# Performance work log

Hardware: AMD Instinct MI355X
Metric: run time of the kernel (lower is better)

Reference implementation:

```python
import jax, jax.numpy as jnp
import numpy as np

B, T, IN_DIM, H_DIM = 64, 512, 512, 1024


def setup_inputs() -> dict:
    key = jax.random.key(0)
    ks = jax.random.split(key, 10)
    s_in = 1.0 / np.sqrt(IN_DIM)
    s_h = 1.0 / np.sqrt(H_DIM)
    return {
        "inputs": jax.random.normal(ks[0], (B, T, IN_DIM), jnp.float32),
        "Wxr": jax.random.normal(ks[1], (H_DIM, IN_DIM), jnp.float32) * s_in,
        "bxr": jax.random.normal(ks[2], (H_DIM,), jnp.float32) * s_in,
        "Whr": jax.random.normal(ks[3], (H_DIM, H_DIM), jnp.float32) * s_h,
        "Wxz": jax.random.normal(ks[4], (H_DIM, IN_DIM), jnp.float32) * s_in,
        "bxz": jax.random.normal(ks[5], (H_DIM,), jnp.float32) * s_in,
        "Whz": jax.random.normal(ks[6], (H_DIM, H_DIM), jnp.float32) * s_h,
        "Wxn": jax.random.normal(ks[7], (H_DIM, IN_DIM), jnp.float32) * s_in,
        "bxn": jax.random.normal(ks[8], (H_DIM,), jnp.float32) * s_in,
        "Whn": jax.random.normal(ks[9], (H_DIM, H_DIM), jnp.float32) * s_h,
    }


def reference(inputs, Wxr, bxr, Whr, Wxz, bxz, Whz, Wxn, bxn, Whn):
    # Precompute all input projections in batched GEMMs: [B,T,H]
    xr = jnp.einsum("bti,hi->bth", inputs, Wxr) + bxr
    xz = jnp.einsum("bti,hi->bth", inputs, Wxz) + bxz
    xn = jnp.einsum("bti,hi->bth", inputs, Wxn) + bxn
    # time-major for scan: [T,B,H]
    xs = (xr.transpose(1, 0, 2), xz.transpose(1, 0, 2), xn.transpose(1, 0, 2))

    def step(h, x):
        xr_t, xz_t, xn_t = x
        r = jax.nn.sigmoid(xr_t + h @ Whr.T)
        z = jax.nn.sigmoid(xz_t + h @ Whz.T)
        n = jnp.tanh(xn_t + r * (h @ Whn.T))
        h_new = (1.0 - z) * n + z * h
        return h_new, h_new

    h0 = jnp.zeros((inputs.shape[0], Wxr.shape[0]), inputs.dtype)
    h_last, hs = jax.lax.scan(step, h0, xs)
    hidden_states = hs.transpose(1, 0, 2)  # [B,T,H] (batch_first)
    # dropout p=0 -> identity
    return (h_last, hidden_states)
```

## Files before the change

kernel.cpp:

```cpp
#include <hip/hip_runtime.h>

typedef __attribute__((ext_vector_type(8))) short short8;
typedef __attribute__((ext_vector_type(4))) float f32x4;

#define TT 512
#define HD 1024
#define BD 64
#define NWG 256

union U16B { short8 s; unsigned long long u[2]; };

__device__ __forceinline__ unsigned short f2bf(float f) {
  unsigned u = __float_as_uint(f);
  u += 0x7fffu + ((u >> 16) & 1u);
  return (unsigned short)(u >> 16);
}

__global__ void prep_xt(const float* __restrict__ x, short8* __restrict__ XT) {
  const int bid = blockIdx.x;
  const int b = bid >> 9;
  const int t = bid & 511;
  const int tid = threadIdx.x;
  const float* src = x + ((size_t)(b * TT + t)) * 512 + tid * 8;
  const f32x4* s4 = (const f32x4*)src;
  f32x4 lo = s4[0], hi = s4[1];
  short8 o;
#pragma unroll
  for (int j = 0; j < 4; ++j) {
    o[j] = (short)f2bf(lo[j]);
    o[4 + j] = (short)f2bf(hi[j]);
  }
  const int bt = b >> 4, m = b & 15, ks = tid >> 2, q = tid & 3;
  XT[(((size_t)bt * TT + t) * 16 + ks) * 64 + q * 16 + m] = o;
}

__global__ __launch_bounds__(256, 1) void gru_main(
    const float* __restrict__ Wxr, const float* __restrict__ bxr,
    const float* __restrict__ Whr,
    const float* __restrict__ Wxz, const float* __restrict__ bxz,
    const float* __restrict__ Whz,
    const float* __restrict__ Wxn, const float* __restrict__ bxn,
    const float* __restrict__ Whn,
    const short8* __restrict__ XT, short* __restrict__ HF,
    unsigned* __restrict__ bar, float* __restrict__ out) {
  extern __shared__ char lds[];
  short8* wh = (short8*)lds;
  short8* wx = (short8*)(lds + 98304);
  float* red = (float*)(lds + 147456);

  const int wg = blockIdx.x;
  const int bt = wg & 3;
  const int ct = wg >> 2;
  const int c0 = ct << 4;
  const int tid = threadIdx.x;
  const int wv = tid >> 6;
  const int lane = tid & 63;

  for (int idx = tid; idx < 3 * 32 * 64; idx += 256) {
    const int g = idx >> 11, rem = idx & 2047, ks = rem >> 6, ln = rem & 63;
    const float* W = (g == 0) ? Whr : (g == 1) ? Whz : Whn;
    const float* src = W + (size_t)(c0 + (ln & 15)) * HD + ks * 32 + (ln >> 4) * 8;
    short8 v;
#pragma unroll
    for (int j = 0; j < 8; ++j) v[j] = (short)f2bf(src[j]);
    wh[idx] = v;
  }
  for (int idx = tid; idx < 3 * 16 * 64; idx += 256) {
    const int g = idx >> 10, rem = idx & 1023, ks = rem >> 6, ln = rem & 63;
    const float* W = (g == 0) ? Wxr : (g == 1) ? Wxz : Wxn;
    const float* src = W + (size_t)(c0 + (ln & 15)) * 512 + ks * 32 + (ln >> 4) * 8;
    short8 v;
#pragma unroll
    for (int j = 0; j < 8; ++j) v[j] = (short)f2bf(src[j]);
    wx[idx] = v;
  }
  __syncthreads();

  const int c_off = tid & 15, b_off = tid >> 4;
  const int c = c0 + c_off;
  const int b = (bt << 4) + b_off;
  const float br_ = bxr[c], bz_ = bxz[c], bn_ = bxn[c];
  float h_old = 0.f;

  const int hf_elem = (((bt * 32 + (c >> 5)) * 64) + ((c >> 3) & 3) * 16 + b_off) * 8 + (c & 7);
  const int rl = ((b_off >> 2) << 4) + c_off;
  const int rr = b_off & 3;

  unsigned* flags = bar + bt * 256;
  const unsigned long long* fl =
      (const unsigned long long*)(flags + lane * 4);

  float* out_hlast = out;
  float* out_hidden = out + BD * HD;

  for (int t = 0; t < TT; ++t) {
    const int p = t & 1;

    const short8* xrd = XT + (((size_t)bt * TT + t) * 16 + (wv << 2)) * 64 + lane;
    short8 xa[4];
#pragma unroll
    for (int kk = 0; kk < 4; ++kk) xa[kk] = xrd[kk * 64];

    f32x4 aR = {0.f, 0.f, 0.f, 0.f};
    f32x4 aZ = {0.f, 0.f, 0.f, 0.f};
    f32x4 aNh = {0.f, 0.f, 0.f, 0.f};
    f32x4 aNx = {0.f, 0.f, 0.f, 0.f};
#pragma unroll
    for (int kk = 0; kk < 4; ++kk) {
      const int ks = (wv << 2) + kk;
      aR = __builtin_amdgcn_mfma_f32_16x16x32_bf16(xa[kk], wx[(0 * 16 + ks) * 64 + lane], aR, 0, 0, 0);
      aZ = __builtin_amdgcn_mfma_f32_16x16x32_bf16(xa[kk], wx[(1 * 16 + ks) * 64 + lane], aZ, 0, 0, 0);
      aNx = __builtin_amdgcn_mfma_f32_16x16x32_bf16(xa[kk], wx[(2 * 16 + ks) * 64 + lane], aNx, 0, 0, 0);
    }

    if (t) {
      const unsigned tt = (unsigned)t;
      for (;;) {
        unsigned long long a0 = __hip_atomic_load(fl, __ATOMIC_RELAXED, __HIP_MEMORY_SCOPE_AGENT);
        unsigned long long a1 = __hip_atomic_load(fl + 1, __ATOMIC_RELAXED, __HIP_MEMORY_SCOPE_AGENT);
        const unsigned f0 = (unsigned)a0, f1 = (unsigned)(a0 >> 32);
        const unsigned f2 = (unsigned)a1, f3 = (unsigned)(a1 >> 32);
        const int ok = (f0 >= tt) & (f1 >= tt) & (f2 >= tt) & (f3 >= tt);
        if (__all(ok)) break;
      }
    }

    const unsigned long long* hfu = (const unsigned long long*)(HF + p * 65536);
    U16B ha[8];
#pragma unroll
    for (int kk = 0; kk < 8; ++kk) {
      const size_t u = (size_t)(bt * 32 + (wv << 3) + kk) * 64 + lane;
      ha[kk].u[0] = __hip_atomic_load(hfu + u * 2, __ATOMIC_RELAXED, __HIP_MEMORY_SCOPE_AGENT);
      ha[kk].u[1] = __hip_atomic_load(hfu + u * 2 + 1, __ATOMIC_RELAXED, __HIP_MEMORY_SCOPE_AGENT);
    }
#pragma unroll
    for (int kk = 0; kk < 8; ++kk) {
      const int ks = (wv << 3) + kk;
      aR = __builtin_amdgcn_mfma_f32_16x16x32_bf16(ha[kk].s, wh[(0 * 32 + ks) * 64 + lane], aR, 0, 0, 0);
      aZ = __builtin_amdgcn_mfma_f32_16x16x32_bf16(ha[kk].s, wh[(1 * 32 + ks) * 64 + lane], aZ, 0, 0, 0);
      aNh = __builtin_amdgcn_mfma_f32_16x16x32_bf16(ha[kk].s, wh[(2 * 32 + ks) * 64 + lane], aNh, 0, 0, 0);
    }

    {
      f32x4* r4 = (f32x4*)red;
      r4[(0 * 4 + wv) * 64 + lane] = aR;
      r4[(1 * 4 + wv) * 64 + lane] = aZ;
      r4[(2 * 4 + wv) * 64 + lane] = aNh;
      r4[(3 * 4 + wv) * 64 + lane] = aNx;
    }
    __syncthreads();
    float sR = 0.f, sZ = 0.f, sNh = 0.f, sNx = 0.f;
#pragma unroll
    for (int v = 0; v < 4; ++v) {
      sR += red[((0 * 4 + v) * 64 + rl) * 4 + rr];
      sZ += red[((1 * 4 + v) * 64 + rl) * 4 + rr];
      sNh += red[((2 * 4 + v) * 64 + rl) * 4 + rr];
      sNx += red[((3 * 4 + v) * 64 + rl) * 4 + rr];
    }

    const float r = 1.f / (1.f + __expf(-(sR + br_)));
    const float z = 1.f / (1.f + __expf(-(sZ + bz_)));
    float pre_n = sNx + bn_ + r * sNh;
    pre_n = fminf(fmaxf(pre_n, -30.f), 30.f);
    const float e2 = __expf(2.f * pre_n);
    const float n = (e2 - 1.f) / (e2 + 1.f);
    const float hn = (1.f - z) * n + z * h_old;
    h_old = hn;

    if (t < TT - 1) {
      __hip_atomic_store((unsigned short*)(HF + ((t + 1) & 1) * 65536 + hf_elem),
                         f2bf(hn), __ATOMIC_RELAXED, __HIP_MEMORY_SCOPE_AGENT);
      asm volatile("s_waitcnt vmcnt(0)" ::: "memory");
      if (lane == 0) {
        __hip_atomic_store(flags + ct * 4 + wv, (unsigned)(t + 1),
                           __ATOMIC_RELAXED, __HIP_MEMORY_SCOPE_AGENT);
      }
      out_hidden[((size_t)b * TT + t) * HD + c] = hn;
    } else {
      out_hidden[((size_t)b * TT + t) * HD + c] = hn;
      out_hlast[(size_t)b * HD + c] = hn;
    }
  }
}

extern "C" void kernel_launch(void* const* d_in, const int* in_sizes, int n_in,
                              void* d_out, int out_size, void* d_ws, size_t ws_size,
                              hipStream_t stream) {
  const float* inputs = (const float*)d_in[0];
  const float* Wxr = (const float*)d_in[1];
  const float* bxr = (const float*)d_in[2];
  const float* Whr = (const float*)d_in[3];
  const float* Wxz = (const float*)d_in[4];
  const float* bxz = (const float*)d_in[5];
  const float* Whz = (const float*)d_in[6];
  const float* Wxn = (const float*)d_in[7];
  const float* bxn = (const float*)d_in[8];
  const float* Whn = (const float*)d_in[9];
  float* out = (float*)d_out;

  char* ws = (char*)d_ws;
  short8* XT = (short8*)ws;
  short* HF = (short*)(ws + 33554432);
  unsigned* bar = (unsigned*)(ws + 33554432 + 262144);

  hipMemsetAsync(bar, 0, 4096, stream);
  hipMemsetAsync(HF, 0, 131072, stream);
  prep_xt<<<dim3(64 * 512), dim3(64), 0, stream>>>(inputs, XT);

  (void)hipFuncSetAttribute((const void*)gru_main,
                            hipFuncAttributeMaxDynamicSharedMemorySize, 163840);
  gru_main<<<dim3(NWG), dim3(256), 163840, stream>>>(
      Wxr, bxr, Whr, Wxz, bxz, Whz, Wxn, bxn, Whn, XT, HF, bar, out);
}
```

Baseline: 1.654 ms.

## Embed step tags in hidden-state words to replace separate flag barrier

Each 64-bit hidden-state slot now carries two bf16 values plus the timestep tag, so consumers poll the data itself instead of separate flag words. This removes the producer's vmcnt wait and the flag store, and it lets the h loads be issued before the input-projection MFMAs. The cost is four times more exchange memory, a shuffle to pack pairs, and an extra __syncthreads to protect the reduction buffer. If any tag mismatches, the whole fragment is reloaded, which can add polling traffic.

```diff
diff --git a/kernel.cpp b/kernel.cpp
--- a/kernel.cpp
+++ b/kernel.cpp
@@ -2,13 +2,14 @@
 
 typedef __attribute__((ext_vector_type(8))) short short8;
 typedef __attribute__((ext_vector_type(4))) float f32x4;
+typedef __attribute__((ext_vector_type(4))) unsigned int u32x4;
 
 #define TT 512
 #define HD 1024
 #define BD 64
 #define NWG 256
 
-union U16B { short8 s; unsigned long long u[2]; };
+union FRAG { u32x4 d; short8 s; };
 
 __device__ __forceinline__ unsigned short f2bf(float f) {
   unsigned u = __float_as_uint(f);
@@ -34,6 +35,8 @@
   XT[(((size_t)bt * TT + t) * 16 + ks) * 64 + q * 16 + m] = o;
 }
 
+#define PARQ ((size_t)(4 * 32 * 64 * 4))
+
 __global__ __launch_bounds__(256, 1) void gru_main(
     const float* __restrict__ Wxr, const float* __restrict__ bxr,
     const float* __restrict__ Whr,
@@ -41,8 +44,8 @@
     const float* __restrict__ Whz,
     const float* __restrict__ Wxn, const float* __restrict__ bxn,
     const float* __restrict__ Whn,
-    const short8* __restrict__ XT, short* __restrict__ HF,
-    unsigned* __restrict__ bar, float* __restrict__ out) {
+    const short8* __restrict__ XT, unsigned long long* __restrict__ HF,
+    float* __restrict__ out) {
   extern __shared__ char lds[];
   short8* wh = (short8*)lds;
   short8* wx = (short8*)(lds + 98304);
@@ -82,19 +85,29 @@
   const float br_ = bxr[c], bz_ = bxz[c], bn_ = bxn[c];
   float h_old = 0.f;
 
-  const int hf_elem = (((bt * 32 + (c >> 5)) * 64) + ((c >> 3) & 3) * 16 + b_off) * 8 + (c & 7);
   const int rl = ((b_off >> 2) << 4) + c_off;
   const int rr = b_off & 3;
 
-  unsigned* flags = bar + bt * 256;
-  const unsigned long long* fl =
-      (const unsigned long long*)(flags + lane * 4);
+  const size_t prod_li =
+      ((size_t)(bt * 32 + (c >> 5)) * 64 + ((c >> 3) & 3) * 16 + b_off) * 4 +
+      ((c & 7) >> 1);
+  const unsigned long long* cons_b =
+      HF + ((size_t)(bt * 32 + (wv << 3)) * 64 + lane) * 4;
 
   float* out_hlast = out;
   float* out_hidden = out + BD * HD;
 
   for (int t = 0; t < TT; ++t) {
     const int p = t & 1;
+    const unsigned long long* cb = cons_b + (size_t)p * PARQ;
+
+    unsigned long long L[8][4];
+#pragma unroll
+    for (int kk = 0; kk < 8; ++kk)
+#pragma unroll
+      for (int j = 0; j < 4; ++j)
+        L[kk][j] = __hip_atomic_load(cb + kk * 256 + j, __ATOMIC_RELAXED,
+                                     __HIP_MEMORY_SCOPE_AGENT);
 
     const short8* xrd = XT + (((size_t)bt * TT + t) * 16 + (wv << 2)) * 64 + lane;
     short8 xa[4];
@@ -113,32 +126,34 @@
       aNx = __builtin_amdgcn_mfma_f32_16x16x32_bf16(xa[kk], wx[(2 * 16 + ks) * 64 + lane], aNx, 0, 0, 0);
     }
 
-    if (t) {
-      const unsigned tt = (unsigned)t;
+    {
+      const unsigned tt_ = (unsigned)t;
       for (;;) {
-        unsigned long long a0 = __hip_atomic_load(fl, __ATOMIC_RELAXED, __HIP_MEMORY_SCOPE_AGENT);
-        unsigned long long a1 = __hip_atomic_load(fl + 1, __ATOMIC_RELAXED, __HIP_MEMORY_SCOPE_AGENT);
-        const unsigned f0 = (unsigned)a0, f1 = (unsigned)(a0 >> 32);
-        const unsigned f2 = (unsigned)a1, f3 = (unsigned)(a1 >> 32);
-        const int ok = (f0 >= tt) & (f1 >= tt) & (f2 >= tt) & (f3 >= tt);
-        if (__all(ok)) break;
+        unsigned bad = 0;
+#pragma unroll
+        for (int kk = 0; kk < 8; ++kk)
+#pragma unroll
+          for (int j = 0; j < 4; ++j)
+            bad |= ((unsigned)(L[kk][j] >> 32)) ^ tt_;
+        if (__all(bad == 0)) break;
+#pragma unroll
+        for (int kk = 0; kk < 8; ++kk)
+#pragma unroll
+          for (int j = 0; j < 4; ++j)
+            L[kk][j] = __hip_atomic_load(cb + kk * 256 + j, __ATOMIC_RELAXED,
+                                         __HIP_MEMORY_SCOPE_AGENT);
       }
     }
 
-    const unsigned long long* hfu = (const unsigned long long*)(HF + p * 65536);
-    U16B ha[8];
 #pragma unroll
     for (int kk = 0; kk < 8; ++kk) {
-      const size_t u = (size_t)(bt * 32 + (wv << 3) + kk) * 64 + lane;
-      ha[kk].u[0] = __hip_atomic_load(hfu + u * 2, __ATOMIC_RELAXED, __HIP_MEMORY_SCOPE_AGENT);
-      ha[kk].u[1] = __hip_atomic_load(hfu + u * 2 + 1, __ATOMIC_RELAXED, __HIP_MEMORY_SCOPE_AGENT);
-    }
-#pragma unroll
-    for (int kk = 0; kk < 8; ++kk) {
+      FRAG f;
+      f.d = (u32x4){(unsigned)L[kk][0], (unsigned)L[kk][1],
+                    (unsigned)L[kk][2], (unsigned)L[kk][3]};
       const int ks = (wv << 3) + kk;
-      aR = __builtin_amdgcn_mfma_f32_16x16x32_bf16(ha[kk].s, wh[(0 * 32 + ks) * 64 + lane], aR, 0, 0, 0);
-      aZ = __builtin_amdgcn_mfma_f32_16x16x32_bf16(ha[kk].s, wh[(1 * 32 + ks) * 64 + lane], aZ, 0, 0, 0);
-      aNh = __builtin_amdgcn_mfma_f32_16x16x32_bf16(ha[kk].s, wh[(2 * 32 + ks) * 64 + lane], aNh, 0, 0, 0);
+      aR = __builtin_amdgcn_mfma_f32_16x16x32_bf16(f.s, wh[(0 * 32 + ks) * 64 + lane], aR, 0, 0, 0);
+      aZ = __builtin_amdgcn_mfma_f32_16x16x32_bf16(f.s, wh[(1 * 32 + ks) * 64 + lane], aZ, 0, 0, 0);
+      aNh = __builtin_amdgcn_mfma_f32_16x16x32_bf16(f.s, wh[(2 * 32 + ks) * 64 + lane], aNh, 0, 0, 0);
     }
 
     {
@@ -157,6 +172,7 @@
       sNh += red[((2 * 4 + v) * 64 + rl) * 4 + rr];
       sNx += red[((3 * 4 + v) * 64 + rl) * 4 + rr];
     }
+    __syncthreads();
 
     const float r = 1.f / (1.f + __expf(-(sR + br_)));
     const float z = 1.f / (1.f + __expf(-(sZ + bz_)));
@@ -167,12 +183,15 @@
     const float hn = (1.f - z) * n + z * h_old;
     h_old = hn;
 
+    const unsigned hb = f2bf(hn);
+    const unsigned hb_hi = (unsigned)__shfl_down((int)hb, 1);
+
     if (t < TT - 1) {
-      __hip_atomic_store((unsigned short*)(HF + ((t + 1) & 1) * 65536 + hf_elem),
-                         f2bf(hn), __ATOMIC_RELAXED, __HIP_MEMORY_SCOPE_AGENT);
-      asm volatile("s_waitcnt vmcnt(0)" ::: "memory");
-      if (lane == 0) {
-        __hip_atomic_store(flags + ct * 4 + wv, (unsigned)(t + 1),
+      if (!(c_off & 1)) {
+        const unsigned long long val =
+            (unsigned long long)(hb | (hb_hi << 16)) |
+            ((unsigned long long)(unsigned)(t + 1) << 32);
+        __hip_atomic_store(HF + (size_t)((t + 1) & 1) * PARQ + prod_li, val,
                            __ATOMIC_RELAXED, __HIP_MEMORY_SCOPE_AGENT);
       }
       out_hidden[((size_t)b * TT + t) * HD + c] = hn;
@@ -200,15 +219,13 @@
 
   char* ws = (char*)d_ws;
   short8* XT = (short8*)ws;
-  short* HF = (short*)(ws + 33554432);
-  unsigned* bar = (unsigned*)(ws + 33554432 + 262144);
-
-  hipMemsetAsync(bar, 0, 4096, stream);
-  hipMemsetAsync(HF, 0, 131072, stream);
+  unsigned long long* HF = (unsigned long long*)(ws + 33554432);
+
+  hipMemsetAsync(HF, 0, 524288, stream);
   prep_xt<<<dim3(64 * 512), dim3(64), 0, stream>>>(inputs, XT);
 
   (void)hipFuncSetAttribute((const void*)gru_main,
                             hipFuncAttributeMaxDynamicSharedMemorySize, 163840);
   gru_main<<<dim3(NWG), dim3(256), 163840, stream>>>(
-      Wxr, bxr, Whr, Wxz, bxz, Whz, Wxn, bxn, Whn, XT, HF, bar, out);
-}
+      Wxr, bxr, Whr, Wxz, bxz, Whz, Wxn, bxn, Whn, XT, HF, out);
+}
```

Result: slower. 3.142 ms (+90.0%).

## Rewrite cross-workgroup wait as inline-asm poll-then-load with packed h stores

Applied to the files above, without the earlier changes.

Replaces the C++ flag-polling loop with an inline-assembly loop. Each lane polls one flag with two staggered in-flight loads, then issues the hidden-state dwordx4 loads right after the wait in the same asm block. Hidden-state writes are packed into 32-bit stores via a lane shuffle, halving the number of stores. Wh fragments are preloaded from LDS into registers before the wait, and a second __syncthreads is added to protect the reduction buffer. The goal is lower per-step barrier latency on the serial recurrence, at the cost of more register pressure and fragile hand-written asm.

```diff
diff --git a/kernel.cpp b/kernel.cpp
--- a/kernel.cpp
+++ b/kernel.cpp
@@ -2,13 +2,14 @@
 
 typedef __attribute__((ext_vector_type(8))) short short8;
 typedef __attribute__((ext_vector_type(4))) float f32x4;
+typedef __attribute__((ext_vector_type(4))) unsigned int u32x4;
 
 #define TT 512
 #define HD 1024
 #define BD 64
 #define NWG 256
 
-union U16B { short8 s; unsigned long long u[2]; };
+union FRAG { u32x4 d; short8 s; };
 
 __device__ __forceinline__ unsigned short f2bf(float f) {
   unsigned u = __float_as_uint(f);
@@ -34,6 +35,39 @@
   XT[(((size_t)bt * TT + t) * 16 + ks) * 64 + q * 16 + m] = o;
 }
 
+#define PARB ((size_t)131072)
+
+#define WAIT_AND_LOAD()                                                   \
+  asm volatile(                                                           \
+      "global_load_dword %8, %10, off sc0 sc1\n\t"                        \
+      "s_sleep 4\n\t"                                                     \
+      "global_load_dword %9, %10, off sc0 sc1\n\t"                        \
+      "1:\n\t"                                                            \
+      "s_waitcnt vmcnt(1)\n\t"                                            \
+      "v_cmp_gt_u32 vcc, %11, %8\n\t"                                     \
+      "s_cbranch_vccz 2f\n\t"                                             \
+      "global_load_dword %8, %10, off sc0 sc1\n\t"                        \
+      "s_waitcnt vmcnt(1)\n\t"                                            \
+      "v_cmp_gt_u32 vcc, %11, %9\n\t"                                     \
+      "s_cbranch_vccz 2f\n\t"                                             \
+      "global_load_dword %9, %10, off sc0 sc1\n\t"                        \
+      "s_branch 1b\n\t"                                                   \
+      "2:\n\t"                                                            \
+      "global_load_dwordx4 %0, %12, off sc0 sc1\n\t"                      \
+      "global_load_dwordx4 %1, %12, off offset:1024 sc0 sc1\n\t"          \
+      "global_load_dwordx4 %2, %12, off offset:2048 sc0 sc1\n\t"          \
+      "global_load_dwordx4 %3, %12, off offset:3072 sc0 sc1\n\t"          \
+      "global_load_dwordx4 %4, %13, off sc0 sc1\n\t"                      \
+      "global_load_dwordx4 %5, %13, off offset:1024 sc0 sc1\n\t"          \
+      "global_load_dwordx4 %6, %13, off offset:2048 sc0 sc1\n\t"          \
+      "global_load_dwordx4 %7, %13, off offset:3072 sc0 sc1\n\t"          \
+      "s_waitcnt vmcnt(0)"                                                \
+      : "=&v"(H[0]), "=&v"(H[1]), "=&v"(H[2]), "=&v"(H[3]),               \
+        "=&v"(H[4]), "=&v"(H[5]), "=&v"(H[6]), "=&v"(H[7]),               \
+        "=&v"(f0s), "=&v"(f1s)                                            \
+      : "v"(hint_p), "v"(tt_), "v"(p0), "v"(p1)                           \
+      : "vcc", "memory")
+
 __global__ __launch_bounds__(256, 1) void gru_main(
     const float* __restrict__ Wxr, const float* __restrict__ bxr,
     const float* __restrict__ Whr,
@@ -41,8 +75,8 @@
     const float* __restrict__ Whz,
     const float* __restrict__ Wxn, const float* __restrict__ bxn,
     const float* __restrict__ Whn,
-    const short8* __restrict__ XT, short* __restrict__ HF,
-    unsigned* __restrict__ bar, float* __restrict__ out) {
+    const short8* __restrict__ XT, char* __restrict__ HFc,
+    unsigned* __restrict__ flags, float* __restrict__ out) {
   extern __shared__ char lds[];
   short8* wh = (short8*)lds;
   short8* wx = (short8*)(lds + 98304);
@@ -82,24 +116,37 @@
   const float br_ = bxr[c], bz_ = bxz[c], bn_ = bxn[c];
   float h_old = 0.f;
 
-  const int hf_elem = (((bt * 32 + (c >> 5)) * 64) + ((c >> 3) & 3) * 16 + b_off) * 8 + (c & 7);
   const int rl = ((b_off >> 2) << 4) + c_off;
   const int rr = b_off & 3;
 
-  unsigned* flags = bar + bt * 256;
-  const unsigned long long* fl =
-      (const unsigned long long*)(flags + lane * 4);
+  const size_t prod_byte =
+      ((size_t)((bt * 32 + (c >> 5)) * 64 + ((c >> 3) & 3) * 16 + b_off)) * 16 +
+      (size_t)(c & 7) * 2;
+  unsigned* my_flag = flags + bt * 256 + ct * 4 + wv;
+  const unsigned* hint_p = flags + bt * 256 + (wv << 6) + lane;
+  const char* cons_base =
+      HFc + ((size_t)(bt * 32 + (wv << 3)) * 64 + lane) * 16;
 
   float* out_hlast = out;
   float* out_hidden = out + BD * HD;
 
   for (int t = 0; t < TT; ++t) {
-    const int p = t & 1;
+    const char* cb = cons_base + (size_t)(t & 1) * PARB;
+    const char* p0 = cb;
+    const char* p1 = cb + 4096;
 
     const short8* xrd = XT + (((size_t)bt * TT + t) * 16 + (wv << 2)) * 64 + lane;
     short8 xa[4];
 #pragma unroll
     for (int kk = 0; kk < 4; ++kk) xa[kk] = xrd[kk * 64];
+
+    short8 whf0[8], whf1[8], whf2[8];
+#pragma unroll
+    for (int kk = 0; kk < 8; ++kk) {
+      whf0[kk] = wh[(0 * 32 + (wv << 3) + kk) * 64 + lane];
+      whf1[kk] = wh[(1 * 32 + (wv << 3) + kk) * 64 + lane];
+      whf2[kk] = wh[(2 * 32 + (wv << 3) + kk) * 64 + lane];
+    }
 
     f32x4 aR = {0.f, 0.f, 0.f, 0.f};
     f32x4 aZ = {0.f, 0.f, 0.f, 0.f};
@@ -113,32 +160,18 @@
       aNx = __builtin_amdgcn_mfma_f32_16x16x32_bf16(xa[kk], wx[(2 * 16 + ks) * 64 + lane], aNx, 0, 0, 0);
     }
 
-    if (t) {
-      const unsigned tt = (unsigned)t;
-      for (;;) {
-        unsigned long long a0 = __hip_atomic_load(fl, __ATOMIC_RELAXED, __HIP_MEMORY_SCOPE_AGENT);
-        unsigned long long a1 = __hip_atomic_load(fl + 1, __ATOMIC_RELAXED, __HIP_MEMORY_SCOPE_AGENT);
-        const unsigned f0 = (unsigned)a0, f1 = (unsigned)(a0 >> 32);
-        const unsigned f2 = (unsigned)a1, f3 = (unsigned)(a1 >> 32);
-        const int ok = (f0 >= tt) & (f1 >= tt) & (f2 >= tt) & (f3 >= tt);
-        if (__all(ok)) break;
-      }
-    }
-
-    const unsigned long long* hfu = (const unsigned long long*)(HF + p * 65536);
-    U16B ha[8];
+    u32x4 H[8];
+    unsigned f0s, f1s;
+    const unsigned tt_ = (unsigned)t;
+    WAIT_AND_LOAD();
+
 #pragma unroll
     for (int kk = 0; kk < 8; ++kk) {
-      const size_t u = (size_t)(bt * 32 + (wv << 3) + kk) * 64 + lane;
-      ha[kk].u[0] = __hip_atomic_load(hfu + u * 2, __ATOMIC_RELAXED, __HIP_MEMORY_SCOPE_AGENT);
-      ha[kk].u[1] = __hip_atomic_load(hfu + u * 2 + 1, __ATOMIC_RELAXED, __HIP_MEMORY_SCOPE_AGENT);
-    }
-#pragma unroll
-    for (int kk = 0; kk < 8; ++kk) {
-      const int ks = (wv << 3) + kk;
-      aR = __builtin_amdgcn_mfma_f32_16x16x32_bf16(ha[kk].s, wh[(0 * 32 + ks) * 64 + lane], aR, 0, 0, 0);
-      aZ = __builtin_amdgcn_mfma_f32_16x16x32_bf16(ha[kk].s, wh[(1 * 32 + ks) * 64 + lane], aZ, 0, 0, 0);
-      aNh = __builtin_amdgcn_mfma_f32_16x16x32_bf16(ha[kk].s, wh[(2 * 32 + ks) * 64 + lane], aNh, 0, 0, 0);
+      FRAG f;
+      f.d = H[kk];
+      aR = __builtin_amdgcn_mfma_f32_16x16x32_bf16(f.s, whf0[kk], aR, 0, 0, 0);
+      aZ = __builtin_amdgcn_mfma_f32_16x16x32_bf16(f.s, whf1[kk], aZ, 0, 0, 0);
+      aNh = __builtin_amdgcn_mfma_f32_16x16x32_bf16(f.s, whf2[kk], aNh, 0, 0, 0);
     }
 
     {
@@ -157,6 +190,7 @@
       sNh += red[((2 * 4 + v) * 64 + rl) * 4 + rr];
       sNx += red[((3 * 4 + v) * 64 + rl) * 4 + rr];
     }
+    __syncthreads();
 
     const float r = 1.f / (1.f + __expf(-(sR + br_)));
     const float z = 1.f / (1.f + __expf(-(sZ + bz_)));
@@ -167,13 +201,19 @@
     const float hn = (1.f - z) * n + z * h_old;
     h_old = hn;
 
+    const unsigned hb = f2bf(hn);
+    const unsigned hb_hi = (unsigned)__shfl_down((int)hb, 1);
+
     if (t < TT - 1) {
-      __hip_atomic_store((unsigned short*)(HF + ((t + 1) & 1) * 65536 + hf_elem),
-                         f2bf(hn), __ATOMIC_RELAXED, __HIP_MEMORY_SCOPE_AGENT);
+      if (!(c_off & 1)) {
+        __hip_atomic_store(
+            (unsigned*)(HFc + (size_t)((t + 1) & 1) * PARB + prod_byte),
+            hb | (hb_hi << 16), __ATOMIC_RELAXED, __HIP_MEMORY_SCOPE_AGENT);
+      }
       asm volatile("s_waitcnt vmcnt(0)" ::: "memory");
       if (lane == 0) {
-        __hip_atomic_store(flags + ct * 4 + wv, (unsigned)(t + 1),
-                           __ATOMIC_RELAXED, __HIP_MEMORY_SCOPE_AGENT);
+        __hip_atomic_store(my_flag, (unsigned)(t + 1), __ATOMIC_RELAXED,
+                           __HIP_MEMORY_SCOPE_AGENT);
       }
       out_hidden[((size_t)b * TT + t) * HD + c] = hn;
     } else {
@@ -200,15 +240,14 @@
 
   char* ws = (char*)d_ws;
   short8* XT = (short8*)ws;
-  short* HF = (short*)(ws + 33554432);
-  unsigned* bar = (unsigned*)(ws + 33554432 + 262144);
-
-  hipMemsetAsync(bar, 0, 4096, stream);
-  hipMemsetAsync(HF, 0, 131072, stream);
+  char* HF = ws + 33554432;
+  unsigned* flags = (unsigned*)(ws + 33554432 + 262144);
+
+  hipMemsetAsync(HF, 0, 262144 + 4096, stream);
   prep_xt<<<dim3(64 * 512), dim3(64), 0, stream>>>(inputs, XT);
 
   (void)hipFuncSetAttribute((const void*)gru_main,
                             hipFuncAttributeMaxDynamicSharedMemorySize, 163840);
   gru_main<<<dim3(NWG), dim3(256), 163840, stream>>>(
-      Wxr, bxr, Whr, Wxz, bxz, Whz, Wxn, bxn, Whn, XT, HF, bar, out);
-}
+      Wxr, bxr, Whr, Wxz, bxz, Whz, Wxn, bxn, Whn, XT, HF, flags, out);
+}
```

New measurement: 1.513 ms. -8.5%, faster.
